# Optimization experiments

Hardware: AMD Instinct MI355X
Metric: run time of the kernel (lower is better)

## Reference

```python
import jax, jax.numpy as jnp
import numpy as np

B, SEQ, DIM, HEADS = 2, 2048, 512, 8
HD = DIM // HEADS
RANK, DFF = 128, 1024
TAU_MEM, TAU_ADAPT, SLOPE, EPS = 0.99, 0.95, 25.0, 1e-6
THRESH, ADAPT_STRENGTH = 0.5, 0.1
TREE_LEVELS = int(np.log2(SEQ))  # 11


def rmsnorm(x, w, eps=EPS):
    return x * jax.lax.rsqrt(jnp.mean(x * x, axis=-1, keepdims=True) + eps) * w


def rope_cos_sin(seq, hd):
    inv = 1.0 / (10000.0 ** (jnp.arange(0, hd, 2, dtype=jnp.float32) / hd))
    f = jnp.arange(seq, dtype=jnp.float32)[:, None] * inv[None, :]  # [S, hd/2]
    emb = jnp.concatenate([f, f], axis=-1)  # [S, hd]
    return jnp.cos(emb), jnp.sin(emb)


def apply_rope(x, cos, sin):
    # x: [B, H, S, hd]; rotate-half formulation
    x1, x2 = jnp.split(x, 2, axis=-1)
    return x * cos + jnp.concatenate([-x2, x1], axis=-1) * sin


def setup_inputs() -> dict:
    key = jax.random.key(0)
    ks = jax.random.split(key, 12)
    w = lambda k, shape, fan: (jax.random.normal(k, shape, jnp.float32) / np.sqrt(fan))
    return {
        "x": jax.random.normal(ks[0], (B, SEQ, DIM), jnp.float32),
        "norm_w": jnp.ones((DIM,), jnp.float32),
        "wq": w(ks[1], (DIM, DIM), DIM),
        "wk": w(ks[2], (DIM, DIM), DIM),
        "wv": w(ks[3], (DIM, DIM), DIM),
        "wo": w(ks[4], (DIM, DIM), DIM),
        "lat_w": w(ks[5], (SEQ, SEQ), SEQ),
        "bt": jnp.full((DIM,), THRESH, jnp.float32),
        "as_w": jnp.full((DIM,), ADAPT_STRENGTH, jnp.float32),
        "gate_w": w(ks[6], (DIM, DIM), DIM),
        "tnorm1_w": jnp.ones((DIM,), jnp.float32),
        "tnorm2_w": jnp.ones((DIM,), jnp.float32),
        "ffn_norm_w": jnp.ones((DIM,), jnp.float32),
        "u_w": w(ks[7], (DIM, RANK), DIM),
        "v_w": w(ks[8], (RANK, 2 * DFF), RANK),
        "down_w": w(ks[9], (DFF, DIM), DFF),
    }


def reference(x, norm_w, wq, wk, wv, wo, lat_w, bt, as_w, gate_w,
              tnorm1_w, tnorm2_w, ffn_norm_w, u_w, v_w, down_w):
    Bx, S, D = x.shape
    # --- pre-norm + QKV projections (base_proj) ---
    h = rmsnorm(x, norm_w)
    q = (h @ wq.T).reshape(Bx, S, HEADS, HD).transpose(0, 2, 1, 3)  # [B,H,S,hd]
    k = (h @ wk.T).reshape(Bx, S, HEADS, HD).transpose(0, 2, 1, 3)
    v = (h @ wv.T).reshape(Bx, S, HEADS, HD).transpose(0, 2, 1, 3)
    # --- RoPE ---
    cos, sin = rope_cos_sin(S, HD)
    q = apply_rope(q, cos, sin)
    k = apply_rope(k, cos, sin)
    # --- causal self-attention ---
    scores = jnp.einsum("bhqd,bhkd->bhqk", q, k) / np.sqrt(HD)
    causal = jnp.tril(jnp.ones((S, S), bool))
    scores = jnp.where(causal, scores, jnp.float32(-1e9))
    attn = jnp.einsum("bhqk,bhkd->bhqd", jax.nn.softmax(scores, axis=-1), v)
    attn = attn.transpose(0, 2, 1, 3).reshape(Bx, S, D) @ wo.T
    # --- causal lateral mixing across sequence ---
    mixed = jnp.einsum("ts,bsd->btd", jnp.tril(lat_w), attn)
    # --- ALIF spiking recurrence over the sequence (soft surrogate spike) ---
    def alif_step(carry, i_t):
        vmem, ad = carry
        vmem = TAU_MEM * vmem + i_t
        th = bt + as_w * ad
        spike = jax.nn.sigmoid(SLOPE * (vmem - th))
        vmem = vmem - spike * th          # soft reset
        ad = TAU_ADAPT * ad + spike        # threshold adaptation
        return (vmem, ad), spike
    init = (jnp.zeros((Bx, D), x.dtype), jnp.zeros((Bx, D), x.dtype))
    _, spikes = jax.lax.scan(alif_step, init, mixed.transpose(1, 0, 2))
    spikes = spikes.transpose(1, 0, 2)  # [B,S,D]
    # --- fused addadd residual ---
    h2 = x + mixed + spikes
    # --- binary-tree cell recursion to a root summary ---
    s = h2
    for _ in range(TREE_LEVELS):
        raw = s[:, 0::2, :] + s[:, 1::2, :]         # pairwise sums (raw_sums)
        res = 0.5 * raw                              # residual / prev_s surrogate
        n = rmsnorm(raw, tnorm1_w)
        g = jax.nn.sigmoid(n @ gate_w.T)
        s = rmsnorm(g * n + (1.0 - g) * res, tnorm2_w)
    h3 = h2 + s[:, 0:1, :]  # broadcast root back over the sequence
    # --- low-rank SwiGLU FFN ---
    hn = rmsnorm(h3, ffn_norm_w)
    up = (hn @ u_w) @ v_w                 # [B,S,2*DFF]
    a, b = jnp.split(up, 2, axis=-1)
    ffn = (jax.nn.silu(a) * b) @ down_w   # [B,S,D]
    return h3 + ffn
```

## Files before the change

kernel.cpp:

```cpp
#include <hip/hip_runtime.h>
#include <math.h>

#define BB 2
#define SS 2048
#define DD 512
#define HH 8
#define HDD 64
#define RANKK 128
#define DFFF 1024

typedef short bf16x8 __attribute__((ext_vector_type(8)));
typedef float f32x4 __attribute__((ext_vector_type(4)));

__device__ __forceinline__ short f2b(float f) {
  union { float f; unsigned u; } v; v.f = f;
  unsigned r = v.u + 0x7FFF + ((v.u >> 16) & 1);
  return (short)(r >> 16);
}
__device__ __forceinline__ float b2f(short s) {
  union { unsigned u; float f; } v; v.u = ((unsigned)(unsigned short)s) << 16;
  return v.f;
}

__device__ __forceinline__ void gll16(const void* g, void* l) {
  __builtin_amdgcn_global_load_lds(
      (const __attribute__((address_space(1))) unsigned int*)g,
      (__attribute__((address_space(3))) unsigned int*)l, 16, 0, 0);
}

__device__ __forceinline__ float wsum(float v) {
#pragma unroll
  for (int off = 32; off > 0; off >>= 1) v += __shfl_xor(v, off, 64);
  return v;
}

__global__ void splitw(const float* __restrict__ in, short* __restrict__ hi,
                       short* __restrict__ lo, int n) {
  int i = (blockIdx.x * 256 + threadIdx.x) * 4;
  if (i >= n) return;
  float4 v = *(const float4*)(in + i);
  short4 h4, l4;
  h4.x = f2b(v.x); l4.x = f2b(v.x - b2f(h4.x));
  h4.y = f2b(v.y); l4.y = f2b(v.y - b2f(h4.y));
  h4.z = f2b(v.z); l4.z = f2b(v.z - b2f(h4.z));
  h4.w = f2b(v.w); l4.w = f2b(v.w - b2f(h4.w));
  *(short4*)(hi + i) = h4;
  *(short4*)(lo + i) = l4;
}

__global__ void cvtb(const float* __restrict__ in, short* __restrict__ out, int n) {
  int i = (blockIdx.x * 256 + threadIdx.x) * 4;
  if (i >= n) return;
  float4 v = *(const float4*)(in + i);
  short4 o; o.x = f2b(v.x); o.y = f2b(v.y); o.z = f2b(v.z); o.w = f2b(v.w);
  *(short4*)(out + i) = o;
}

__global__ void transp_cvt(const float* __restrict__ in, short* __restrict__ out,
                           int R, int C) {
  __shared__ float t[32][33];
  int c0 = blockIdx.x * 32, r0 = blockIdx.y * 32;
#pragma unroll
  for (int i = 0; i < 4; i++) {
    int idx = threadIdx.x + i * 256;
    int r = idx >> 5, c = idx & 31;
    t[r][c] = in[(size_t)(r0 + r) * C + c0 + c];
  }
  __syncthreads();
#pragma unroll
  for (int i = 0; i < 4; i++) {
    int idx = threadIdx.x + i * 256;
    int cc = idx >> 5, rr = idx & 31;
    out[(size_t)(c0 + cc) * R + r0 + rr] = f2b(t[rr][cc]);
  }
}

__global__ void rmsnorm_hl(const float* __restrict__ x, const float* __restrict__ w,
                           short* __restrict__ oh, short* __restrict__ ol, int rows) {
  int wid = blockIdx.x * 4 + (threadIdx.x >> 6);
  int lane = threadIdx.x & 63;
  if (wid >= rows) return;
  const float* xp = x + (size_t)wid * DD + lane * 8;
  float4 a = *(const float4*)xp;
  float4 b = *(const float4*)(xp + 4);
  float ss = a.x*a.x + a.y*a.y + a.z*a.z + a.w*a.w
           + b.x*b.x + b.y*b.y + b.z*b.z + b.w*b.w;
  ss = wsum(ss);
  float r = rsqrtf(ss * (1.0f / DD) + 1e-6f);
  const float* wp = w + lane * 8;
  float4 wa = *(const float4*)wp, wb = *(const float4*)(wp + 4);
  float o8[8] = {a.x*r*wa.x, a.y*r*wa.y, a.z*r*wa.z, a.w*r*wa.w,
                 b.x*r*wb.x, b.y*r*wb.y, b.z*r*wb.z, b.w*r*wb.w};
  short hv[8], lv[8];
#pragma unroll
  for (int i = 0; i < 8; i++) { hv[i] = f2b(o8[i]); lv[i] = f2b(o8[i] - b2f(hv[i])); }
  short* op = oh + (size_t)wid * DD + lane * 8;
  short* lp = ol + (size_t)wid * DD + lane * 8;
  *(short4*)op = make_short4(hv[0], hv[1], hv[2], hv[3]);
  *(short4*)(op + 4) = make_short4(hv[4], hv[5], hv[6], hv[7]);
  *(short4*)lp = make_short4(lv[0], lv[1], lv[2], lv[3]);
  *(short4*)(lp + 4) = make_short4(lv[4], lv[5], lv[6], lv[7]);
}

template <bool SPL, int OM, bool ROPE>
__global__ __launch_bounds__(256) void ggemm(const short* __restrict__ Ah_g,
                                             const short* __restrict__ Al_g,
                                             const short* __restrict__ Bh_g,
                                             const short* __restrict__ Bl_g,
                                             const float* __restrict__ ADD,
                                             void* __restrict__ C, void* __restrict__ C2,
                                             int M, int N, int K) {
  __shared__ short Ahs[128 * 32];
  __shared__ short Bhs[128 * 32];
  __shared__ short Als[SPL ? 128 * 32 : 8];
  __shared__ short Bls[SPL ? 128 * 32 : 8];
  const int tid = threadIdx.x, l = tid & 63, w = tid >> 6;
  const int wr = (w >> 1) * 64, wc = (w & 1) * 64;
  const int bm = blockIdx.y * 128, bn = blockIdx.x * 128;
  f32x4 acc[4][4] = {};
  for (int k0 = 0; k0 < K; k0 += 32) {
#pragma unroll
    for (int p = 0; p < 2; p++) {
      int row = p * 64 + (tid >> 2), g = tid & 3;
      int swz = (g ^ ((row >> 1) & 3)) * 8;
      gll16(Ah_g + (size_t)(bm + row) * K + k0 + swz, Ahs + p * 2048 + tid * 8);
      gll16(Bh_g + (size_t)(bn + row) * K + k0 + swz, Bhs + p * 2048 + tid * 8);
      if (SPL) {
        gll16(Al_g + (size_t)(bm + row) * K + k0 + swz, Als + p * 2048 + tid * 8);
        gll16(Bl_g + (size_t)(bn + row) * K + k0 + swz, Bls + p * 2048 + tid * 8);
      }
    }
    __syncthreads();
    bf16x8 ah[4], bh[4], al[4], bl[4];
#pragma unroll
    for (int m = 0; m < 4; m++) {
      int r = wr + m * 16 + (l & 15);
      int go = (((l >> 4) ^ ((r >> 1) & 3)) << 3);
      ah[m] = *(const bf16x8*)(Ahs + r * 32 + go);
      if (SPL) al[m] = *(const bf16x8*)(Als + r * 32 + go);
    }
#pragma unroll
    for (int n = 0; n < 4; n++) {
      int r = wc + n * 16 + (l & 15);
      int go = (((l >> 4) ^ ((r >> 1) & 3)) << 3);
      bh[n] = *(const bf16x8*)(Bhs + r * 32 + go);
      if (SPL) bl[n] = *(const bf16x8*)(Bls + r * 32 + go);
    }
#pragma unroll
    for (int m = 0; m < 4; m++)
#pragma unroll
      for (int n = 0; n < 4; n++) {
        acc[m][n] = __builtin_amdgcn_mfma_f32_16x16x32_bf16(ah[m], bh[n], acc[m][n], 0, 0, 0);
        if (SPL) {
          acc[m][n] = __builtin_amdgcn_mfma_f32_16x16x32_bf16(ah[m], bl[n], acc[m][n], 0, 0, 0);
          acc[m][n] = __builtin_amdgcn_mfma_f32_16x16x32_bf16(al[m], bh[n], acc[m][n], 0, 0, 0);
        }
      }
    __syncthreads();
  }
  const int ll = l & 15, lg4 = (l >> 4) * 4;
  if (ROPE) {
#pragma unroll
    for (int m = 0; m < 4; m++)
#pragma unroll
      for (int n = 0; n < 2; n++) {
        int i_ = n * 16 + ll;
        float inv = exp2f(-(float)i_ * (13.287712379549449f / 32.0f));
#pragma unroll
        for (int j = 0; j < 4; j++) {
          int gm = bm + wr + m * 16 + lg4 + j;
          int s = gm & (SS - 1);
          float ang = (float)s * inv;
          float sn, cs;
          sincosf(ang, &sn, &cs);
          float v1 = acc[m][n][j], v2 = acc[m][n + 2][j];
          acc[m][n][j]     = v1 * cs - v2 * sn;
          acc[m][n + 2][j] = v2 * cs + v1 * sn;
        }
      }
  }
#pragma unroll
  for (int m = 0; m < 4; m++)
#pragma unroll
    for (int n = 0; n < 4; n++) {
      int gn = bn + wc + n * 16 + ll;
#pragma unroll
      for (int j = 0; j < 4; j++) {
        int gm = bm + wr + m * 16 + lg4 + j;
        if (gm >= M || gn >= N) continue;
        float v = acc[m][n][j];
        if (OM == 0) {
          ((float*)C)[(size_t)gm * N + gn] = v;
        } else if (OM == 1) {
          ((short*)C)[(size_t)gm * N + gn] = f2b(v);
        } else if (OM == 6) {
          size_t off = (size_t)gm * N + gn;
          ((float*)C)[off] = v + ADD[off];
        } else {
          short hi = f2b(v);
          short lo = f2b(v - b2f(hi));
          int b = gm >> 11, s = gm & (SS - 1);
          int hh2 = gn >> 6, d = gn & 63;
          size_t off;
          if (OM == 2)      off = (((size_t)(b * HH + hh2)) * SS + s) * 64 + d;
          else if (OM == 3) off = (((size_t)(b * HH + hh2)) * 64 + d) * SS + s;
          else              off = ((size_t)(b * DD) + gn) * SS + s;
          ((short*)C)[off] = hi;
          ((short*)C2)[off] = lo;
        }
      }
    }
}

__global__ __launch_bounds__(256) void qkv_g(const short* __restrict__ Ah_g,
                                             const short* __restrict__ Al_g,
                                             const short* __restrict__ wh0, const short* __restrict__ wl0,
                                             const short* __restrict__ wh1, const short* __restrict__ wl1,
                                             const short* __restrict__ wh2, const short* __restrict__ wl2,
                                             short* __restrict__ c0h, short* __restrict__ c0l,
                                             short* __restrict__ c1h, short* __restrict__ c1l,
                                             short* __restrict__ c2h, short* __restrict__ c2l) {
  const int z = blockIdx.z;
  const short* Bh_g = (z == 0) ? wh0 : (z == 1) ? wh1 : wh2;
  const short* Bl_g = (z == 0) ? wl0 : (z == 1) ? wl1 : wl2;
  short* Ch = (z == 0) ? c0h : (z == 1) ? c1h : c2h;
  short* Cl = (z == 0) ? c0l : (z == 1) ? c1l : c2l;
  const int K = DD;
  __shared__ short Ahs[128 * 32];
  __shared__ short Bhs[128 * 32];
  __shared__ short Als[128 * 32];
  __shared__ short Bls[128 * 32];
  const int tid = threadIdx.x, l = tid & 63, w = tid >> 6;
  const int wr = (w >> 1) * 64, wc = (w & 1) * 64;
  const int bm = blockIdx.y * 128, bn = blockIdx.x * 128;
  f32x4 acc[4][4] = {};
  for (int k0 = 0; k0 < K; k0 += 32) {
#pragma unroll
    for (int p = 0; p < 2; p++) {
      int row = p * 64 + (tid >> 2), g = tid & 3;
      int swz = (g ^ ((row >> 1) & 3)) * 8;
      gll16(Ah_g + (size_t)(bm + row) * K + k0 + swz, Ahs + p * 2048 + tid * 8);
      gll16(Bh_g + (size_t)(bn + row) * K + k0 + swz, Bhs + p * 2048 + tid * 8);
      gll16(Al_g + (size_t)(bm + row) * K + k0 + swz, Als + p * 2048 + tid * 8);
      gll16(Bl_g + (size_t)(bn + row) * K + k0 + swz, Bls + p * 2048 + tid * 8);
    }
    __syncthreads();
    bf16x8 ah[4], bh[4], al[4], bl[4];
#pragma unroll
    for (int m = 0; m < 4; m++) {
      int r = wr + m * 16 + (l & 15);
      int go = (((l >> 4) ^ ((r >> 1) & 3)) << 3);
      ah[m] = *(const bf16x8*)(Ahs + r * 32 + go);
      al[m] = *(const bf16x8*)(Als + r * 32 + go);
    }
#pragma unroll
    for (int n = 0; n < 4; n++) {
      int r = wc + n * 16 + (l & 15);
      int go = (((l >> 4) ^ ((r >> 1) & 3)) << 3);
      bh[n] = *(const bf16x8*)(Bhs + r * 32 + go);
      bl[n] = *(const bf16x8*)(Bls + r * 32 + go);
    }
#pragma unroll
    for (int m = 0; m < 4; m++)
#pragma unroll
      for (int n = 0; n < 4; n++) {
        acc[m][n] = __builtin_amdgcn_mfma_f32_16x16x32_bf16(ah[m], bh[n], acc[m][n], 0, 0, 0);
        acc[m][n] = __builtin_amdgcn_mfma_f32_16x16x32_bf16(ah[m], bl[n], acc[m][n], 0, 0, 0);
        acc[m][n] = __builtin_amdgcn_mfma_f32_16x16x32_bf16(al[m], bh[n], acc[m][n], 0, 0, 0);
      }
    __syncthreads();
  }
  const int ll = l & 15, lg4 = (l >> 4) * 4;
  if (z < 2) {
#pragma unroll
    for (int m = 0; m < 4; m++)
#pragma unroll
      for (int n = 0; n < 2; n++) {
        int i_ = n * 16 + ll;
        float inv = exp2f(-(float)i_ * (13.287712379549449f / 32.0f));
#pragma unroll
        for (int j = 0; j < 4; j++) {
          int gm = bm + wr + m * 16 + lg4 + j;
          int s = gm & (SS - 1);
          float ang = (float)s * inv;
          float sn, cs;
          sincosf(ang, &sn, &cs);
          float v1 = acc[m][n][j], v2 = acc[m][n + 2][j];
          acc[m][n][j]     = v1 * cs - v2 * sn;
          acc[m][n + 2][j] = v2 * cs + v1 * sn;
        }
      }
  }
#pragma unroll
  for (int m = 0; m < 4; m++)
#pragma unroll
    for (int n = 0; n < 4; n++) {
      int gn = bn + wc + n * 16 + ll;
#pragma unroll
      for (int j = 0; j < 4; j++) {
        int gm = bm + wr + m * 16 + lg4 + j;
        float v = acc[m][n][j];
        short hi = f2b(v);
        short lo = f2b(v - b2f(hi));
        int b = gm >> 11, s = gm & (SS - 1);
        int hh2 = gn >> 6, d = gn & 63;
        size_t off = (z < 2) ? ((((size_t)(b * HH + hh2)) * SS + s) * 64 + d)
                             : ((((size_t)(b * HH + hh2)) * 64 + d) * SS + s);
        Ch[off] = hi;
        Cl[off] = lo;
      }
    }
}

__global__ __launch_bounds__(256) void lat_g(const float* __restrict__ lat,
                                             const short* __restrict__ bTh,
                                             const short* __restrict__ bTl,
                                             float* __restrict__ P0,
                                             float* __restrict__ P1) {
  const int zb = blockIdx.z >> 1;
  const int half = blockIdx.z & 1;
  bTh += (size_t)zb * DD * SS;
  bTl += (size_t)zb * DD * SS;
  float* Cc = (half == 0 ? P0 : P1) + (size_t)zb * DD * SS;
  __shared__ short Ah[128 * 32];
  __shared__ short Al[128 * 32];
  __shared__ short Bh[128 * 32];
  __shared__ short Bl[128 * 32];
  const int tid = threadIdx.x, l = tid & 63, w = tid >> 6;
  const int wr = (w >> 1) * 64, wc = (w & 1) * 64;
  const int bm = blockIdx.y * 128, bn = blockIdx.x * 128;
  const int T = blockIdx.y + 1;
  const int h0 = (T + 1) >> 1;
  const int kbeg = (half == 0) ? 0 : h0 * 128;
  const int kend = (half == 0) ? h0 * 128 : T * 128;
  f32x4 acc[4][4] = {};
  const int ll = l & 15, lg4 = (l >> 4) * 4;
  for (int k0 = kbeg; k0 < kend; k0 += 32) {
#pragma unroll
    for (int p = 0; p < 2; p++) {
      int row = p * 64 + (tid >> 2), g = tid & 3;
      int swz = (g ^ ((row >> 1) & 3)) * 8;
      gll16(bTh + (size_t)(bn + row) * SS + k0 + swz, Bh + p * 2048 + tid * 8);
      gll16(bTl + (size_t)(bn + row) * SS + k0 + swz, Bl + p * 2048 + tid * 8);
    }
#pragma unroll
    for (int i = 0; i < 4; i++) {
      int lin = i * 256 + tid;
      int row = lin >> 3, f4 = lin & 7;
      int gr = bm + row;
      float4 v = *(const float4*)(lat + (size_t)gr * SS + k0 + f4 * 4);
      int kc = k0 + f4 * 4;
      if (kc + 0 > gr) v.x = 0.0f;
      if (kc + 1 > gr) v.y = 0.0f;
      if (kc + 2 > gr) v.z = 0.0f;
      if (kc + 3 > gr) v.w = 0.0f;
      int off = row * 32 + (((f4 >> 1) ^ ((row >> 1) & 3)) << 3) + (f4 & 1) * 4;
      short4 hh, lo;
      hh.x = f2b(v.x); lo.x = f2b(v.x - b2f(hh.x));
      hh.y = f2b(v.y); lo.y = f2b(v.y - b2f(hh.y));
      hh.z = f2b(v.z); lo.z = f2b(v.z - b2f(hh.z));
      hh.w = f2b(v.w); lo.w = f2b(v.w - b2f(hh.w));
      *(short4*)(Ah + off) = hh;
      *(short4*)(Al + off) = lo;
    }
    __syncthreads();
    bf16x8 ah[4], bh[4], al[4], bl[4];
#pragma unroll
    for (int m = 0; m < 4; m++) {
      int r = wr + m * 16 + (l & 15);
      int go = (((l >> 4) ^ ((r >> 1) & 3)) << 3);
      ah[m] = *(const bf16x8*)(Ah + r * 32 + go);
      al[m] = *(const bf16x8*)(Al + r * 32 + go);
    }
#pragma unroll
    for (int n = 0; n < 4; n++) {
      int r = wc + n * 16 + (l & 15);
      int go = (((l >> 4) ^ ((r >> 1) & 3)) << 3);
      bh[n] = *(const bf16x8*)(Bh + r * 32 + go);
      bl[n] = *(const bf16x8*)(Bl + r * 32 + go);
    }
#pragma unroll
    for (int m = 0; m < 4; m++)
#pragma unroll
      for (int n = 0; n < 4; n++) {
        acc[m][n] = __builtin_amdgcn_mfma_f32_16x16x32_bf16(ah[m], bh[n], acc[m][n], 0, 0, 0);
        acc[m][n] = __builtin_amdgcn_mfma_f32_16x16x32_bf16(ah[m], bl[n], acc[m][n], 0, 0, 0);
        acc[m][n] = __builtin_amdgcn_mfma_f32_16x16x32_bf16(al[m], bh[n], acc[m][n], 0, 0, 0);
      }
    __syncthreads();
  }
#pragma unroll
  for (int m = 0; m < 4; m++)
#pragma unroll
    for (int n = 0; n < 4; n++) {
      int gn = bn + wc + n * 16 + ll;
#pragma unroll
      for (int j = 0; j < 4; j++) {
        int gm = bm + wr + m * 16 + lg4 + j;
        Cc[(size_t)gn * SS + gm] = acc[m][n][j];
      }
    }
}

__global__ __launch_bounds__(256) void attn_g(const short* __restrict__ qh,
                                              const short* __restrict__ ql,
                                              const short* __restrict__ kh,
                                              const short* __restrict__ kl,
                                              const short* __restrict__ vh,
                                              const short* __restrict__ vl,
                                              short* __restrict__ aho,
                                              short* __restrict__ alo) {
  const int h = blockIdx.y, b = blockIdx.z;
  const int qt = (b == 0) ? (int)blockIdx.x : 31 - (int)blockIdx.x;
  const int q0 = qt * 64;
  const int tid = threadIdx.x, w = tid >> 6, l = tid & 63;
  const int lg = l >> 4, ll = l & 15;
  __shared__ short Kh[64 * 64], Kl[64 * 64];
  __shared__ short Vh[64 * 64], Vl[64 * 64];
  __shared__ short Ph[64 * 64], Pl[64 * 64];
  const size_t bh = (size_t)(b * HH + h);

  const int qr = q0 + w * 16 + ll;
  const short* qbh = qh + (bh * SS + qr) * 64;
  const short* qbl = ql + (bh * SS + qr) * 64;
  bf16x8 qfh[2], qfl[2];
#pragma unroll
  for (int ks = 0; ks < 2; ks++) {
    qfh[ks] = *(const bf16x8*)(qbh + (ks * 4 + lg) * 8);
    qfl[ks] = *(const bf16x8*)(qbl + (ks * 4 + lg) * 8);
  }

  f32x4 o[4] = {};
  float mrow[4] = {-1e30f, -1e30f, -1e30f, -1e30f};
  float lsum[4] = {};
  const int qrow0 = q0 + w * 16 + lg * 4;
  const int ntiles = qt + 1;

  for (int kt = 0; kt < ntiles; kt++) {
#pragma unroll
    for (int p = 0; p < 2; p++) {
      int row = p * 32 + (tid >> 3), g = tid & 7;
      int sw = ((g ^ (row & 7)) << 3);
      size_t krow = (bh * SS + kt * 64 + row) * 64;
      size_t vrow = (bh * 64 + row) * SS + kt * 64;
      gll16(kh + krow + sw, Kh + p * 2048 + tid * 8);
      gll16(kl + krow + sw, Kl + p * 2048 + tid * 8);
      gll16(vh + vrow + sw, Vh + p * 2048 + tid * 8);
      gll16(vl + vrow + sw, Vl + p * 2048 + tid * 8);
    }
    __syncthreads();

    f32x4 sv[4] = {};
#pragma unroll
    for (int nf = 0; nf < 4; nf++) {
      int r = nf * 16 + ll;
#pragma unroll
      for (int ks = 0; ks < 2; ks++) {
        int g = (ks * 4 + lg) ^ (r & 7);
        bf16x8 khf = *(const bf16x8*)(Kh + r * 64 + g * 8);
        bf16x8 klf = *(const bf16x8*)(Kl + r * 64 + g * 8);
        sv[nf] = __builtin_amdgcn_mfma_f32_16x16x32_bf16(qfh[ks], khf, sv[nf], 0, 0, 0);
        sv[nf] = __builtin_amdgcn_mfma_f32_16x16x32_bf16(qfh[ks], klf, sv[nf], 0, 0, 0);
        sv[nf] = __builtin_amdgcn_mfma_f32_16x16x32_bf16(qfl[ks], khf, sv[nf], 0, 0, 0);
      }
    }
#pragma unroll
    for (int nf = 0; nf < 4; nf++) {
      int kpos = kt * 64 + nf * 16 + ll;
#pragma unroll
      for (int j = 0; j < 4; j++) {
        float v = sv[nf][j] * 0.125f;
        sv[nf][j] = (kpos > qrow0 + j) ? -1e30f : v;
      }
    }
    float cf[4];
#pragma unroll
    for (int j = 0; j < 4; j++) {
      float r = fmaxf(fmaxf(sv[0][j], sv[1][j]), fmaxf(sv[2][j], sv[3][j]));
      r = fmaxf(r, __shfl_xor(r, 1)); r = fmaxf(r, __shfl_xor(r, 2));
      r = fmaxf(r, __shfl_xor(r, 4)); r = fmaxf(r, __shfl_xor(r, 8));
      float mn = fmaxf(mrow[j], r);
      cf[j] = __expf(mrow[j] - mn);
      mrow[j] = mn;
    }
    float ps[4] = {};
#pragma unroll
    for (int nf = 0; nf < 4; nf++)
#pragma unroll
      for (int j = 0; j < 4; j++) {
        float p = __expf(sv[nf][j] - mrow[j]);
        sv[nf][j] = p;
        ps[j] += p;
      }
#pragma unroll
    for (int j = 0; j < 4; j++) {
      float r = ps[j];
      r += __shfl_xor(r, 1); r += __shfl_xor(r, 2);
      r += __shfl_xor(r, 4); r += __shfl_xor(r, 8);
      lsum[j] = lsum[j] * cf[j] + r;
    }
#pragma unroll
    for (int nf = 0; nf < 4; nf++)
#pragma unroll
      for (int j = 0; j < 4; j++) o[nf][j] *= cf[j];
#pragma unroll
    for (int nf = 0; nf < 4; nf++)
#pragma unroll
      for (int j = 0; j < 4; j++) {
        int rowP = w * 16 + lg * 4 + j;
        int col = nf * 16 + ll;
        int off = rowP * 64 + (((col >> 3) ^ (rowP & 7)) << 3) + (col & 7);
        float p = sv[nf][j];
        short hi = f2b(p);
        Ph[off] = hi;
        Pl[off] = f2b(p - b2f(hi));
      }
    __syncthreads();
    bf16x8 pfh[2], pfl[2];
    {
      int rowA = w * 16 + ll;
#pragma unroll
      for (int ks = 0; ks < 2; ks++) {
        int g = (ks * 4 + lg) ^ (rowA & 7);
        pfh[ks] = *(const bf16x8*)(Ph + rowA * 64 + g * 8);
        pfl[ks] = *(const bf16x8*)(Pl + rowA * 64 + g * 8);
      }
    }
#pragma unroll
    for (int nf = 0; nf < 4; nf++) {
      int r = nf * 16 + ll;
#pragma unroll
      for (int ks = 0; ks < 2; ks++) {
        int g = (ks * 4 + lg) ^ (r & 7);
        bf16x8 vhf = *(const bf16x8*)(Vh + r * 64 + g * 8);
        bf16x8 vlf = *(const bf16x8*)(Vl + r * 64 + g * 8);
        o[nf] = __builtin_amdgcn_mfma_f32_16x16x32_bf16(pfh[ks], vhf, o[nf], 0, 0, 0);
        o[nf] = __builtin_amdgcn_mfma_f32_16x16x32_bf16(pfh[ks], vlf, o[nf], 0, 0, 0);
        o[nf] = __builtin_amdgcn_mfma_f32_16x16x32_bf16(pfl[ks], vhf, o[nf], 0, 0, 0);
      }
    }
    __syncthreads();
  }
  float inv[4];
#pragma unroll
  for (int j = 0; j < 4; j++) inv[j] = 1.0f / lsum[j];
#pragma unroll
  for (int nf = 0; nf < 4; nf++)
#pragma unroll
    for (int j = 0; j < 4; j++) {
      float v = o[nf][j] * inv[j];
      short hi = f2b(v);
      size_t off = ((size_t)(b * SS + qrow0 + j)) * DD + h * HDD + nf * 16 + ll;
      aho[off] = hi;
      alo[off] = f2b(v - b2f(hi));
    }
}

#define ACH 32
__global__ __launch_bounds__(64, 1) void tsa_alif4(const float* __restrict__ P0,
                                                   const float* __restrict__ P1,
                                                   const float* __restrict__ bt,
                                                   const float* __restrict__ asw,
                                                   float* __restrict__ spikesT) {
  int tid = blockIdx.x * 64 + threadIdx.x;
  int b = tid >> 9, d = tid & 511;
  const float btd = bt[d], asd = asw[d];
  const float C = 36.06737602222409f;
  const float bt36 = btd * C, as36 = asd * C;
  const float bt99 = 0.99f * btd, as99 = 0.99f * asd;
  const size_t base = ((size_t)(b * DD + d)) * SS;
  const float* p0 = P0 + base;
  const float* p1 = P1 + base;
  float* sp = spikesT + base;
  float mA[ACH], mB[ACH], sO[ACH];
#pragma unroll
  for (int k = 0; k < ACH / 4; k++) {
    float4 a = *(const float4*)(p0 + k * 4);
    float4 bq = *(const float4*)(p1 + k * 4);
    mA[k*4+0] = a.x + bq.x; mA[k*4+1] = a.y + bq.y;
    mA[k*4+2] = a.z + bq.z; mA[k*4+3] = a.w + bq.w;
  }
#pragma unroll
  for (int k = 0; k < ACH / 4; k++) {
    float4 a = *(const float4*)(p0 + ACH + k * 4);
    float4 bq = *(const float4*)(p1 + ACH + k * 4);
    mB[k*4+0] = a.x + bq.x; mB[k*4+1] = a.y + bq.y;
    mB[k*4+2] = a.z + bq.z; mB[k*4+3] = a.w + bq.w;
  }
  float vR = mA[0];
  float ad = 0.0f;
  for (int t0 = 0; t0 < SS; t0 += 2 * ACH) {
    bool more = (t0 + 2 * ACH < SS);
#pragma unroll
    for (int j = 0; j < ACH; j++) {
      float thC = fmaf(ad, as36, bt36);
      float th99 = fmaf(ad, as99, bt99);
      float arg = fmaf(vR, -C, thC);
      float e = exp2f(arg);
      float s = __builtin_amdgcn_rcpf(1.0f + e);
      float mn = (j + 1 < ACH) ? mA[j + 1] : mB[0];
      float pre = fmaf(0.99f, vR, mn);
      sO[j] = s;
      vR = fmaf(-th99, s, pre);
      ad = fmaf(0.95f, ad, s);
    }
#pragma unroll
    for (int k = 0; k < ACH / 4; k++) *(float4*)(sp + t0 + k * 4) = *(const float4*)&sO[k * 4];
    if (more) {
#pragma unroll
      for (int k = 0; k < ACH / 4; k++) {
        float4 a = *(const float4*)(p0 + t0 + 2 * ACH + k * 4);
        float4 bq = *(const float4*)(p1 + t0 + 2 * ACH + k * 4);
        mA[k*4+0] = a.x + bq.x; mA[k*4+1] = a.y + bq.y;
        mA[k*4+2] = a.z + bq.z; mA[k*4+3] = a.w + bq.w;
      }
    }
#pragma unroll
    for (int j = 0; j < ACH; j++) {
      float thC = fmaf(ad, as36, bt36);
      float th99 = fmaf(ad, as99, bt99);
      float arg = fmaf(vR, -C, thC);
      float e = exp2f(arg);
      float s = __builtin_amdgcn_rcpf(1.0f + e);
      float mn = (j + 1 < ACH) ? mB[j + 1] : (more ? mA[0] : 0.0f);
      float pre = fmaf(0.99f, vR, mn);
      sO[j] = s;
      vR = fmaf(-th99, s, pre);
      ad = fmaf(0.95f, ad, s);
    }
#pragma unroll
    for (int k = 0; k < ACH / 4; k++) *(float4*)(sp + t0 + ACH + k * 4) = *(const float4*)&sO[k * 4];
    if (more) {
#pragma unroll
      for (int k = 0; k < ACH / 4; k++) {
        float4 a = *(const float4*)(p0 + t0 + 3 * ACH + k * 4);
        float4 bq = *(const float4*)(p1 + t0 + 3 * ACH + k * 4);
        mB[k*4+0] = a.x + bq.x; mB[k*4+1] = a.y + bq.y;
        mB[k*4+2] = a.z + bq.z; mB[k*4+3] = a.w + bq.w;
      }
    }
  }
}

__global__ __launch_bounds__(256) void fuse_h2(const float* __restrict__ x,
                                               const float* __restrict__ P0,
                                               const float* __restrict__ P1,
                                               const float* __restrict__ spikesT,
                                               float* __restrict__ h2) {
  const int s0 = blockIdx.x * 64, d0 = blockIdx.y * 64, b = blockIdx.z;
  __shared__ float t[64][65];
#pragma unroll
  for (int k = 0; k < 4; k++) {
    int dl = threadIdx.x >> 2;
    int sl = (threadIdx.x & 3) * 16 + k * 4;
    size_t off = ((size_t)(b * DD + d0 + dl)) * SS + s0 + sl;
    float4 m0 = *(const float4*)(P0 + off);
    float4 m1 = *(const float4*)(P1 + off);
    float4 sv = *(const float4*)(spikesT + off);
    t[dl][sl + 0] = m0.x + m1.x + sv.x;
    t[dl][sl + 1] = m0.y + m1.y + sv.y;
    t[dl][sl + 2] = m0.z + m1.z + sv.z;
    t[dl][sl + 3] = m0.w + m1.w + sv.w;
  }
  __syncthreads();
#pragma unroll
  for (int k = 0; k < 4; k++) {
    int sl = threadIdx.x >> 2;
    int dl = (threadIdx.x & 3) * 16 + k * 4;
    size_t off = ((size_t)(b * SS + s0 + sl)) * DD + d0 + dl;
    float4 xv = *(const float4*)(x + off);
    float4 o;
    o.x = xv.x + t[dl + 0][sl];
    o.y = xv.y + t[dl + 1][sl];
    o.z = xv.z + t[dl + 2][sl];
    o.w = xv.w + t[dl + 3][sl];
    *(float4*)(h2 + off) = o;
  }
}

__global__ void tree_reduce_b(const float* __restrict__ sin_, const float* __restrict__ tn1,
                              short* __restrict__ nb, int Sn) {
  int wid = blockIdx.x * 4 + (threadIdx.x >> 6);
  int lane = threadIdx.x & 63;
  int rows = BB * Sn;
  if (wid >= rows) return;
  int b = wid / Sn, j = wid - b * Sn;
  const float* r0 = sin_ + ((size_t)(b * 2 * Sn + 2 * j)) * DD + lane * 8;
  const float* r1 = r0 + DD;
  float4 a0 = *(const float4*)r0, a1 = *(const float4*)(r0 + 4);
  float4 b0 = *(const float4*)r1, b1 = *(const float4*)(r1 + 4);
  float ra[8] = {a0.x + b0.x, a0.y + b0.y, a0.z + b0.z, a0.w + b0.w,
                 a1.x + b1.x, a1.y + b1.y, a1.z + b1.z, a1.w + b1.w};
  float ss = 0.0f;
#pragma unroll
  for (int i = 0; i < 8; i++) ss += ra[i] * ra[i];
  ss = wsum(ss);
  float rms = rsqrtf(ss * (1.0f / DD) + 1e-6f);
  const float* wp = tn1 + lane * 8;
  float4 wa = *(const float4*)wp, wb = *(const float4*)(wp + 4);
  float wv8[8] = {wa.x, wa.y, wa.z, wa.w, wb.x, wb.y, wb.z, wb.w};
  short* np = nb + (size_t)wid * DD + lane * 8;
  short4 n0, n1;
  n0.x = f2b(ra[0]*rms*wv8[0]); n0.y = f2b(ra[1]*rms*wv8[1]);
  n0.z = f2b(ra[2]*rms*wv8[2]); n0.w = f2b(ra[3]*rms*wv8[3]);
  n1.x = f2b(ra[4]*rms*wv8[4]); n1.y = f2b(ra[5]*rms*wv8[5]);
  n1.z = f2b(ra[6]*rms*wv8[6]); n1.w = f2b(ra[7]*rms*wv8[7]);
  *(short4*)np = n0;
  *(short4*)(np + 4) = n1;
}

__global__ void tree_combine_b(const float* __restrict__ g, const short* __restrict__ nb,
                               const float* __restrict__ sin_, const float* __restrict__ tn2,
                               float* __restrict__ sout, int Sn) {
  int wid = blockIdx.x * 4 + (threadIdx.x >> 6);
  int lane = threadIdx.x & 63;
  int rows = BB * Sn;
  if (wid >= rows) return;
  int b = wid / Sn, j = wid - b * Sn;
  const float* r0 = sin_ + ((size_t)(b * 2 * Sn + 2 * j)) * DD + lane * 8;
  const float* r1 = r0 + DD;
  float4 a0 = *(const float4*)r0, a1 = *(const float4*)(r0 + 4);
  float4 b0 = *(const float4*)r1, b1 = *(const float4*)(r1 + 4);
  float res[8] = {0.5f*(a0.x + b0.x), 0.5f*(a0.y + b0.y), 0.5f*(a0.z + b0.z), 0.5f*(a0.w + b0.w),
                  0.5f*(a1.x + b1.x), 0.5f*(a1.y + b1.y), 0.5f*(a1.z + b1.z), 0.5f*(a1.w + b1.w)};
  size_t base = (size_t)wid * DD + lane * 8;
  float t[8];
  float ss = 0.0f;
#pragma unroll
  for (int i = 0; i < 8; i++) {
    float gg = 1.0f / (1.0f + expf(-g[base + i]));
    float tv = gg * b2f(nb[base + i]) + (1.0f - gg) * res[i];
    t[i] = tv;
    ss += tv * tv;
  }
  ss = wsum(ss);
  float rms = rsqrtf(ss * (1.0f / DD) + 1e-6f);
#pragma unroll
  for (int i = 0; i < 8; i++) sout[base + i] = t[i] * rms * tn2[lane * 8 + i];
}

__global__ void h3hn_b(const float* __restrict__ h2, const float* __restrict__ root,
                       const float* __restrict__ fw, float* __restrict__ h3,
                       short* __restrict__ hn) {
  int wid = blockIdx.x * 4 + (threadIdx.x >> 6);
  int lane = threadIdx.x & 63;
  int b = wid >> 11;
  size_t base = (size_t)wid * DD + lane * 8;
  const float* rp = root + (size_t)b * DD + lane * 8;
  float t[8];
  float ss = 0.0f;
#pragma unroll
  for (int i = 0; i < 8; i++) {
    float tv = h2[base + i] + rp[i];
    t[i] = tv;
    ss += tv * tv;
    h3[base + i] = tv;
  }
  ss = wsum(ss);
  float rms = rsqrtf(ss * (1.0f / DD) + 1e-6f);
#pragma unroll
  for (int i = 0; i < 8; i++) hn[base + i] = f2b(t[i] * rms * fw[lane * 8 + i]);
}

__global__ __launch_bounds__(256) void upgate_g(const short* __restrict__ A,
                                                const short* __restrict__ Bv,
                                                short* __restrict__ ffa) {
  __shared__ short Ahs[128 * 32];
  __shared__ short B1s[128 * 32];
  __shared__ short B2s[128 * 32];
  const int tid = threadIdx.x, l = tid & 63, w = tid >> 6;
  const int wr = (w >> 1) * 64, wc = (w & 1) * 64;
  const int bm = blockIdx.y * 128, bn = blockIdx.x * 128;
  f32x4 acc1[4][4] = {}, acc2[4][4] = {};
  for (int k0 = 0; k0 < RANKK; k0 += 32) {
#pragma unroll
    for (int p = 0; p < 2; p++) {
      int row = p * 64 + (tid >> 2), g = tid & 3;
      int swz = (g ^ ((row >> 1) & 3)) * 8;
      gll16(A + (size_t)(bm + row) * RANKK + k0 + swz, Ahs + p * 2048 + tid * 8);
      gll16(Bv + (size_t)(bn + row) * RANKK + k0 + swz, B1s + p * 2048 + tid * 8);
      gll16(Bv + (size_t)(DFFF + bn + row) * RANKK + k0 + swz, B2s + p * 2048 + tid * 8);
    }
    __syncthreads();
    bf16x8 ah[4], b1[4], b2[4];
#pragma unroll
    for (int m = 0; m < 4; m++) {
      int r = wr + m * 16 + (l & 15);
      int go = (((l >> 4) ^ ((r >> 1) & 3)) << 3);
      ah[m] = *(const bf16x8*)(Ahs + r * 32 + go);
    }
#pragma unroll
    for (int n = 0; n < 4; n++) {
      int r = wc + n * 16 + (l & 15);
      int go = (((l >> 4) ^ ((r >> 1) & 3)) << 3);
      b1[n] = *(const bf16x8*)(B1s + r * 32 + go);
      b2[n] = *(const bf16x8*)(B2s + r * 32 + go);
    }
#pragma unroll
    for (int m = 0; m < 4; m++)
#pragma unroll
      for (int n = 0; n < 4; n++) {
        acc1[m][n] = __builtin_amdgcn_mfma_f32_16x16x32_bf16(ah[m], b1[n], acc1[m][n], 0, 0, 0);
        acc2[m][n] = __builtin_amdgcn_mfma_f32_16x16x32_bf16(ah[m], b2[n], acc2[m][n], 0, 0, 0);
      }
    __syncthreads();
  }
#pragma unroll
  for (int m = 0; m < 4; m++)
#pragma unroll
    for (int n = 0; n < 4; n++) {
      int gn = bn + wc + n * 16 + (l & 15);
#pragma unroll
      for (int j = 0; j < 4; j++) {
        int gm = bm + wr + m * 16 + (l >> 4) * 4 + j;
        float a = acc1[m][n][j];
        float s = a / (1.0f + __expf(-a));
        ffa[(size_t)gm * DFFF + gn] = f2b(s * acc2[m][n][j]);
      }
    }
}

extern "C" void kernel_launch(void* const* d_in, const int* in_sizes, int n_in,
                              void* d_out, int out_size, void* d_ws, size_t ws_size,
                              hipStream_t stream) {
  const float* x   = (const float*)d_in[0];
  const float* nw  = (const float*)d_in[1];
  const float* wq  = (const float*)d_in[2];
  const float* wk  = (const float*)d_in[3];
  const float* wv  = (const float*)d_in[4];
  const float* wo  = (const float*)d_in[5];
  const float* lat = (const float*)d_in[6];
  const float* btp = (const float*)d_in[7];
  const float* asw = (const float*)d_in[8];
  const float* gw  = (const float*)d_in[9];
  const float* tn1 = (const float*)d_in[10];
  const float* tn2 = (const float*)d_in[11];
  const float* fnw = (const float*)d_in[12];
  const float* uw  = (const float*)d_in[13];
  const float* vw  = (const float*)d_in[14];
  const float* dw  = (const float*)d_in[15];
  float* out = (float*)d_out;
  char* W = (char*)d_ws;
  const size_t MB = 1u << 20;

  short* h_hi = (short*)(W);
  short* h_lo = (short*)(W + 4 * MB);
  short* attn_hi = h_hi;
  short* attn_lo = h_lo;
  short* nb = (short*)(W);
  float* gb = (float*)(W + 2 * MB);
  short* q_hi = (short*)(W + 8 * MB);
  short* q_lo = (short*)(W + 12 * MB);
  short* apT_hi = q_hi;
  short* apT_lo = q_lo;
  float* spikesT = (float*)(W + 8 * MB);
  float* s0 = (float*)(W + 8 * MB);
  float* s1 = (float*)(W + 12 * MB);
  short* k_hi = (short*)(W + 16 * MB);
  short* k_lo = (short*)(W + 20 * MB);
  float* latP1 = (float*)(W + 16 * MB);
  short* hn = (short*)(W + 16 * MB);
  short* t1 = (short*)(W + 20 * MB);
  short* v_hi = (short*)(W + 24 * MB);
  short* v_lo = (short*)(W + 28 * MB);
  float* h2 = (float*)(W + 24 * MB);
  short* ffa = (short*)(W + 24 * MB);
  float* latP0 = (float*)(W + 32 * MB);
  short* gwb = (short*)(W + 32 * MB);
  short* uwT = gwb + 262144;
  short* vwT = uwT + 65536;
  short* dwT = vwT + 262144;

  short* wqh = (short*)out;
  short* wql = wqh + 262144;
  short* wkh = wql + 262144;
  short* wkl = wkh + 262144;
  short* wvh = wkl + 262144;
  short* wvl = wvh + 262144;
  short* woh = wvl + 262144;
  short* wol = woh + 262144;

  const int rows = BB * SS;

  splitw<<<256, 256, 0, stream>>>(wq, wqh, wql, DD * DD);
  splitw<<<256, 256, 0, stream>>>(wk, wkh, wkl, DD * DD);
  splitw<<<256, 256, 0, stream>>>(wv, wvh, wvl, DD * DD);
  splitw<<<256, 256, 0, stream>>>(wo, woh, wol, DD * DD);

  rmsnorm_hl<<<rows / 4, 256, 0, stream>>>(x, nw, h_hi, h_lo, rows);

  qkv_g<<<dim3(4, 32, 3), 256, 0, stream>>>(h_hi, h_lo,
                                            wqh, wql, wkh, wkl, wvh, wvl,
                                            q_hi, q_lo, k_hi, k_lo, v_hi, v_lo);

  attn_g<<<dim3(32, HH, BB), 256, 0, stream>>>(q_hi, q_lo, k_hi, k_lo, v_hi, v_lo,
                                               attn_hi, attn_lo);

  ggemm<true, 4, false><<<dim3(4, 32), 256, 0, stream>>>(
      attn_hi, attn_lo, woh, wol, nullptr, apT_hi, apT_lo, rows, DD, DD);

  lat_g<<<dim3(4, 16, 4), 256, 0, stream>>>(lat, apT_hi, apT_lo, latP0, latP1);

  tsa_alif4<<<16, 64, 0, stream>>>(latP0, latP1, btp, asw, spikesT);
  fuse_h2<<<dim3(32, 8, 2), 256, 0, stream>>>(x, latP0, latP1, spikesT, h2);

  cvtb<<<256, 256, 0, stream>>>(gw, gwb, DD * DD);
  transp_cvt<<<dim3(4, 16), 256, 0, stream>>>(uw, uwT, DD, RANKK);
  transp_cvt<<<dim3(64, 4), 256, 0, stream>>>(vw, vwT, RANKK, 2 * DFFF);
  transp_cvt<<<dim3(16, 32), 256, 0, stream>>>(dw, dwT, DFFF, DD);

  const float* sin_ = h2;
  for (int lvl = 0; lvl < 11; lvl++) {
    int Sn = 1024 >> lvl;
    int r2 = BB * Sn;
    float* sout = (lvl & 1) ? s1 : s0;
    tree_reduce_b<<<(r2 + 3) / 4, 256, 0, stream>>>(sin_, tn1, nb, Sn);
    ggemm<false, 0, false><<<dim3(4, (r2 + 127) / 128), 256, 0, stream>>>(
        nb, nullptr, gwb, nullptr, nullptr, gb, nullptr, r2, DD, DD);
    tree_combine_b<<<(r2 + 3) / 4, 256, 0, stream>>>(gb, nb, sin_, tn2, sout, Sn);
    sin_ = sout;
  }

  h3hn_b<<<rows / 4, 256, 0, stream>>>(h2, sin_, fnw, out, hn);

  ggemm<false, 1, false><<<dim3(1, 32), 256, 0, stream>>>(
      hn, nullptr, uwT, nullptr, nullptr, t1, nullptr, rows, RANKK, DD);
  upgate_g<<<dim3(8, 32), 256, 0, stream>>>(t1, vwT, ffa);
  ggemm<false, 6, false><<<dim3(4, 32), 256, 0, stream>>>(
      ffa, nullptr, dwT, nullptr, out, out, nullptr, rows, DD, DFFF);
}
```

Baseline: 693.1 us.

## Pre-sum latent partials and stream ALIF inputs through double-buffered LDS

Adds a sum2 kernel that merges the two split-K latent partials into one buffer before the serial ALIF scan, so the scan and fuse_h2 each read one array instead of two. The ALIF kernel now prefetches the next 32-step chunk into double-buffered shared memory with global_load_lds, so the loads can overlap the sequential recurrence instead of being register loads that stall. This costs an extra elementwise pass over the full tensor and a barrier per chunk. The 4-byte LDS loads read strided addresses (one row per thread), so they may coalesce poorly.

Measured after the change: 679.9 us. About the same (-1.9%).

```diff
diff --git a/kernel.cpp b/kernel.cpp
--- a/kernel.cpp
+++ b/kernel.cpp
@@ -26,6 +26,11 @@
   __builtin_amdgcn_global_load_lds(
       (const __attribute__((address_space(1))) unsigned int*)g,
       (__attribute__((address_space(3))) unsigned int*)l, 16, 0, 0);
+}
+__device__ __forceinline__ void gll4(const void* g, void* l) {
+  __builtin_amdgcn_global_load_lds(
+      (const __attribute__((address_space(1))) unsigned int*)g,
+      (__attribute__((address_space(3))) unsigned int*)l, 4, 0, 0);
 }
 
 __device__ __forceinline__ float wsum(float v) {
@@ -54,6 +59,15 @@
   float4 v = *(const float4*)(in + i);
   short4 o; o.x = f2b(v.x); o.y = f2b(v.y); o.z = f2b(v.z); o.w = f2b(v.w);
   *(short4*)(out + i) = o;
+}
+
+__global__ void sum2(const float* __restrict__ a, const float* __restrict__ bq,
+                     float* __restrict__ o) {
+  int i = (blockIdx.x * 256 + threadIdx.x) * 4;
+  float4 va = *(const float4*)(a + i);
+  float4 vb = *(const float4*)(bq + i);
+  float4 vo = {va.x + vb.x, va.y + vb.y, va.z + vb.z, va.w + vb.w};
+  *(float4*)(o + i) = vo;
 }
 
 __global__ void transp_cvt(const float* __restrict__ in, short* __restrict__ out,
@@ -557,40 +571,37 @@
 }
 
 #define ACH 32
-__global__ __launch_bounds__(64, 1) void tsa_alif4(const float* __restrict__ P0,
-                                                   const float* __restrict__ P1,
+__global__ __launch_bounds__(64, 1) void tsa_alif5(const float* __restrict__ mixedT,
                                                    const float* __restrict__ bt,
                                                    const float* __restrict__ asw,
                                                    float* __restrict__ spikesT) {
-  int tid = blockIdx.x * 64 + threadIdx.x;
-  int b = tid >> 9, d = tid & 511;
+  __shared__ float lds[2][ACH * 64];
+  const int t = threadIdx.x;
+  const int tid = blockIdx.x * 64 + t;
+  const int b = tid >> 9, d = tid & 511;
   const float btd = bt[d], asd = asw[d];
   const float C = 36.06737602222409f;
   const float bt36 = btd * C, as36 = asd * C;
   const float bt99 = 0.99f * btd, as99 = 0.99f * asd;
   const size_t base = ((size_t)(b * DD + d)) * SS;
-  const float* p0 = P0 + base;
-  const float* p1 = P1 + base;
+  const float* mp = mixedT + base;
   float* sp = spikesT + base;
-  float mA[ACH], mB[ACH], sO[ACH];
-#pragma unroll
-  for (int k = 0; k < ACH / 4; k++) {
-    float4 a = *(const float4*)(p0 + k * 4);
-    float4 bq = *(const float4*)(p1 + k * 4);
-    mA[k*4+0] = a.x + bq.x; mA[k*4+1] = a.y + bq.y;
-    mA[k*4+2] = a.z + bq.z; mA[k*4+3] = a.w + bq.w;
-  }
-#pragma unroll
-  for (int k = 0; k < ACH / 4; k++) {
-    float4 a = *(const float4*)(p0 + ACH + k * 4);
-    float4 bq = *(const float4*)(p1 + ACH + k * 4);
-    mB[k*4+0] = a.x + bq.x; mB[k*4+1] = a.y + bq.y;
-    mB[k*4+2] = a.z + bq.z; mB[k*4+3] = a.w + bq.w;
-  }
-  float vR = mA[0];
-  float ad = 0.0f;
-  for (int t0 = 0; t0 < SS; t0 += 2 * ACH) {
-    bool more = (t0 + 2 * ACH < SS);
+#pragma unroll
+  for (int j = 0; j < ACH; j++) gll4(mp + j, &lds[0][j * 64]);
+  float vR = 0.0f, ad = 0.0f;
+  for (int c = 0; c < SS / ACH; c++) {
+    const int cur = c & 1;
+    __syncthreads();
+    if (c + 1 < SS / ACH) {
+      const float* q = mp + (c + 1) * ACH;
+#pragma unroll
+      for (int j = 0; j < ACH; j++) gll4(q + j, &lds[cur ^ 1][j * 64]);
+    }
+    float m[ACH];
+#pragma unroll
+    for (int j = 0; j < ACH; j++) m[j] = lds[cur][j * 64 + t];
+    vR += m[0];
+    float sO[ACH];
 #pragma unroll
     for (int j = 0; j < ACH; j++) {
       float thC = fmaf(ad, as36, bt36);
@@ -598,53 +609,20 @@
       float arg = fmaf(vR, -C, thC);
       float e = exp2f(arg);
       float s = __builtin_amdgcn_rcpf(1.0f + e);
-      float mn = (j + 1 < ACH) ? mA[j + 1] : mB[0];
-      float pre = fmaf(0.99f, vR, mn);
       sO[j] = s;
+      float pre = (j + 1 < ACH) ? fmaf(0.99f, vR, m[j + 1]) : (0.99f * vR);
       vR = fmaf(-th99, s, pre);
       ad = fmaf(0.95f, ad, s);
-    }
-#pragma unroll
-    for (int k = 0; k < ACH / 4; k++) *(float4*)(sp + t0 + k * 4) = *(const float4*)&sO[k * 4];
-    if (more) {
-#pragma unroll
-      for (int k = 0; k < ACH / 4; k++) {
-        float4 a = *(const float4*)(p0 + t0 + 2 * ACH + k * 4);
-        float4 bq = *(const float4*)(p1 + t0 + 2 * ACH + k * 4);
-        mA[k*4+0] = a.x + bq.x; mA[k*4+1] = a.y + bq.y;
-        mA[k*4+2] = a.z + bq.z; mA[k*4+3] = a.w + bq.w;
-      }
-    }
-#pragma unroll
-    for (int j = 0; j < ACH; j++) {
-      float thC = fmaf(ad, as36, bt36);
-      float th99 = fmaf(ad, as99, bt99);
-      float arg = fmaf(vR, -C, thC);
-      float e = exp2f(arg);
-      float s = __builtin_amdgcn_rcpf(1.0f + e);
-      float mn = (j + 1 < ACH) ? mB[j + 1] : (more ? mA[0] : 0.0f);
-      float pre = fmaf(0.99f, vR, mn);
-      sO[j] = s;
-      vR = fmaf(-th99, s, pre);
-      ad = fmaf(0.95f, ad, s);
-    }
-#pragma unroll
-    for (int k = 0; k < ACH / 4; k++) *(float4*)(sp + t0 + ACH + k * 4) = *(const float4*)&sO[k * 4];
-    if (more) {
-#pragma unroll
-      for (int k = 0; k < ACH / 4; k++) {
-        float4 a = *(const float4*)(p0 + t0 + 3 * ACH + k * 4);
-        float4 bq = *(const float4*)(p1 + t0 + 3 * ACH + k * 4);
-        mB[k*4+0] = a.x + bq.x; mB[k*4+1] = a.y + bq.y;
-        mB[k*4+2] = a.z + bq.z; mB[k*4+3] = a.w + bq.w;
+      if ((j & 3) == 3) {
+        float4 o4 = {sO[j - 3], sO[j - 2], sO[j - 1], sO[j]};
+        *(float4*)(sp + c * ACH + (j - 3)) = o4;
       }
     }
   }
 }
 
 __global__ __launch_bounds__(256) void fuse_h2(const float* __restrict__ x,
-                                               const float* __restrict__ P0,
-                                               const float* __restrict__ P1,
+                                               const float* __restrict__ mixedT,
                                                const float* __restrict__ spikesT,
                                                float* __restrict__ h2) {
   const int s0 = blockIdx.x * 64, d0 = blockIdx.y * 64, b = blockIdx.z;
@@ -654,13 +632,12 @@
     int dl = threadIdx.x >> 2;
     int sl = (threadIdx.x & 3) * 16 + k * 4;
     size_t off = ((size_t)(b * DD + d0 + dl)) * SS + s0 + sl;
-    float4 m0 = *(const float4*)(P0 + off);
-    float4 m1 = *(const float4*)(P1 + off);
+    float4 mv = *(const float4*)(mixedT + off);
     float4 sv = *(const float4*)(spikesT + off);
-    t[dl][sl + 0] = m0.x + m1.x + sv.x;
-    t[dl][sl + 1] = m0.y + m1.y + sv.y;
-    t[dl][sl + 2] = m0.z + m1.z + sv.z;
-    t[dl][sl + 3] = m0.w + m1.w + sv.w;
+    t[dl][sl + 0] = mv.x + sv.x;
+    t[dl][sl + 1] = mv.y + sv.y;
+    t[dl][sl + 2] = mv.z + sv.z;
+    t[dl][sl + 3] = mv.w + sv.w;
   }
   __syncthreads();
 #pragma unroll
@@ -901,8 +878,10 @@
 
   lat_g<<<dim3(4, 16, 4), 256, 0, stream>>>(lat, apT_hi, apT_lo, latP0, latP1);
 
-  tsa_alif4<<<16, 64, 0, stream>>>(latP0, latP1, btp, asw, spikesT);
-  fuse_h2<<<dim3(32, 8, 2), 256, 0, stream>>>(x, latP0, latP1, spikesT, h2);
+  sum2<<<(BB * DD * SS / 4) / 256, 256, 0, stream>>>(latP0, latP1, latP0);
+
+  tsa_alif5<<<16, 64, 0, stream>>>(latP0, btp, asw, spikesT);
+  fuse_h2<<<dim3(32, 8, 2), 256, 0, stream>>>(x, latP0, spikesT, h2);
 
   cvtb<<<256, 256, 0, stream>>>(gw, gwb, DD * DD);
   transp_cvt<<<dim3(4, 16), 256, 0, stream>>>(uw, uwT, DD, RANKK);
```
